# Kernel optimization log

Hardware: AMD Instinct MI355X
Metric: run time of the kernel (lower is better)

## Reference

```python
import jax, jax.numpy as jnp
import numpy as np

N_NODES = 100000
N_EDGES = 1600000
IN_SIZE = 256
HID = 64
HEADS = 2
OUT_SIZE = 16


def _gat_layer(x, W, a_l, a_r, b, src, dst, n_nodes, heads, feat):
    # x: [N, Din]; W: [Din, H*F]; a_l, a_r: [H, F]; b: [H*F]
    h = (x @ W).reshape(n_nodes, heads, feat)          # [N, H, F]
    el = jnp.sum(h * a_l, axis=-1)                     # [N, H]
    er = jnp.sum(h * a_r, axis=-1)                     # [N, H]
    e = jax.nn.leaky_relu(el[src] + er[dst], 0.2)      # [E, H]
    # segment softmax over incoming edges of each dst node
    m = jax.ops.segment_max(e, dst, num_segments=n_nodes)
    m = jnp.where(jnp.isfinite(m), m, 0.0)             # nodes with no in-edges
    p = jnp.exp(e - m[dst])                            # [E, H]
    s = jax.ops.segment_sum(p, dst, num_segments=n_nodes)
    alpha = p / (s[dst] + 1e-9)                        # [E, H]
    # scatter-add weighted source features
    out = jax.ops.segment_sum(alpha[:, :, None] * h[src], dst, num_segments=n_nodes)
    return out + b.reshape(1, heads, feat)             # [N, H, F]


def setup_inputs() -> dict:
    key = jax.random.key(0)
    ks = jax.random.split(key, 12)
    features = jax.random.normal(ks[0], (N_NODES, IN_SIZE), dtype=jnp.float32)
    src = jax.random.randint(ks[1], (N_EDGES,), 0, N_NODES, dtype=jnp.int32)
    dst = jax.random.randint(ks[2], (N_EDGES,), 0, N_NODES, dtype=jnp.int32)
    s1 = 1.0 / np.sqrt(IN_SIZE)
    s2 = 1.0 / np.sqrt(HID * HEADS)
    W1 = jax.random.normal(ks[3], (IN_SIZE, HEADS * HID), dtype=jnp.float32) * s1
    al1 = jax.random.normal(ks[4], (HEADS, HID), dtype=jnp.float32) * 0.1
    ar1 = jax.random.normal(ks[5], (HEADS, HID), dtype=jnp.float32) * 0.1
    b1 = jnp.zeros((HEADS * HID,), dtype=jnp.float32)
    W2 = jax.random.normal(ks[6], (HEADS * HID, HEADS * HID), dtype=jnp.float32) * s2
    al2 = jax.random.normal(ks[7], (HEADS, HID), dtype=jnp.float32) * 0.1
    ar2 = jax.random.normal(ks[8], (HEADS, HID), dtype=jnp.float32) * 0.1
    b2 = jnp.zeros((HEADS * HID,), dtype=jnp.float32)
    Wl = jax.random.normal(ks[9], (HEADS * HID, OUT_SIZE), dtype=jnp.float32) * s2
    bl = jnp.zeros((OUT_SIZE,), dtype=jnp.float32)
    return {"features": features, "src": src, "dst": dst,
            "W1": W1, "al1": al1, "ar1": ar1, "b1": b1,
            "W2": W2, "al2": al2, "ar2": ar2, "b2": b2,
            "Wl": Wl, "bl": bl}


def reference(features, src, dst, W1, al1, ar1, b1, W2, al2, ar2, b2, Wl, bl):
    n = features.shape[0]
    h = _gat_layer(features, W1, al1, ar1, b1.reshape(HEADS, HID).reshape(-1),
                   src, dst, n, HEADS, HID)
    h = jax.nn.elu(h.reshape(n, HEADS * HID))          # flatten(1) + ELU (dropout: eval)
    h = _gat_layer(h, W2, al2, ar2, b2, src, dst, n, HEADS, HID)
    h = jax.nn.elu(h.reshape(n, HEADS * HID))
    return h @ Wl + bl                                  # [N, OUT_SIZE]
```

## Files before the change

### kernel.cpp

```cpp
#include <hip/hip_runtime.h>
#include <hip/hip_fp16.h>

#define N_NODES 100000
#define N_EDGES 1600000
#define IN_SIZE 256
#define HID 64
#define HEADS 2
#define DMODEL 128
#define OUT_SZ 16

#define BSHIFT 9
#define BNODES 512
#define NB 196
#define CAP 16384
#define EPB 4096

typedef _Float16 f16x4 __attribute__((ext_vector_type(4)));
typedef _Float16 f16x8 __attribute__((ext_vector_type(8)));
typedef float f32x4 __attribute__((ext_vector_type(4)));


__global__ __launch_bounds__(256) void bin_kernel(const int* __restrict__ src,
                                                  const int* __restrict__ dst,
                                                  int* __restrict__ counts,
                                                  int2* __restrict__ bucketbuf, int e) {
    __shared__ int hist[NB];
    __shared__ int base[NB];
    int tid = threadIdx.x;
    int start = blockIdx.x * EPB;
    for (int i = tid; i < NB; i += 256) hist[i] = 0;
    __syncthreads();
    int pack[16];
    #pragma unroll
    for (int i = 0; i < 16; i++) {
        int idx = start + i * 256 + tid;
        int p = -1;
        if (idx < e) {
            int b = dst[idx] >> BSHIFT;
            int r = atomicAdd(&hist[b], 1);
            p = (b << 16) | r;
        }
        pack[i] = p;
    }
    __syncthreads();
    for (int i = tid; i < NB; i += 256)
        base[i] = atomicAdd(&counts[i], hist[i]);
    __syncthreads();
    #pragma unroll
    for (int i = 0; i < 16; i++) {
        int idx = start + i * 256 + tid;
        int p = pack[i];
        if (p >= 0) {
            int b = p >> 16;
            int pos = base[b] + (p & 0xffff);
            if (pos < CAP)
                bucketbuf[(size_t)b * CAP + pos] = make_int2(src[idx], dst[idx]);
        }
    }
}

__global__ void bucket_scan_kernel(const int* __restrict__ counts,
                                   int* __restrict__ bases) {
    __shared__ int lds[256];
    int tid = threadIdx.x;
    int t = (tid < NB) ? min(counts[tid], CAP) : 0;
    lds[tid] = t;
    __syncthreads();
    for (int off = 1; off < 256; off <<= 1) {
        int x = 0;
        if (tid >= off) x = lds[tid - off];
        __syncthreads();
        lds[tid] += x;
        __syncthreads();
    }
    if (tid < NB) bases[tid] = lds[tid] - t;
}


__global__ __launch_bounds__(256) void csr_kernel(const int2* __restrict__ bucketbuf,
                                                  const int* __restrict__ counts,
                                                  const int* __restrict__ bases,
                                                  int* __restrict__ deg,
                                                  int* __restrict__ offs,
                                                  int2* __restrict__ spack, int n) {
    __shared__ int hist[BNODES];
    __shared__ int cursor[BNODES];
    __shared__ int lds[256];
    int b = blockIdx.x;
    int tid = threadIdx.x;
    int cnt = min(counts[b], CAP);
    int base = bases[b];
    int node0 = b << BSHIFT;
    const int2* ebuf = bucketbuf + (size_t)b * CAP;

    hist[tid] = 0;
    hist[tid + 256] = 0;
    __syncthreads();
    for (int i = tid; i < cnt; i += 256)
        atomicAdd(&hist[ebuf[i].y - node0], 1);
    __syncthreads();

    int h0 = hist[2 * tid], h1 = hist[2 * tid + 1];
    lds[tid] = h0 + h1;
    __syncthreads();
    for (int off = 1; off < 256; off <<= 1) {
        int x = 0;
        if (tid >= off) x = lds[tid - off];
        __syncthreads();
        lds[tid] += x;
        __syncthreads();
    }
    int excl = lds[tid] - (h0 + h1);
    cursor[2 * tid] = excl;
    cursor[2 * tid + 1] = excl + h0;
    int g0 = node0 + 2 * tid, g1 = g0 + 1;
    if (g0 < n) { deg[g0] = h0; offs[g0] = base + excl; }
    if (g1 < n) { deg[g1] = h1; offs[g1] = base + excl + h0; }
    __syncthreads();

    for (int i = tid; i < cnt; i += 256) {
        int2 ed = ebuf[i];
        int p = atomicAdd(&cursor[ed.y - node0], 1);
        spack[base + p] = ed;
    }
}


template <int K>
__global__ void wt_kernel(const float* __restrict__ W, _Float16* __restrict__ Wt) {
    int i = blockIdx.x * blockDim.x + threadIdx.x;
    if (i >= 128 * K) return;
    int nr = i / K;
    int k = i - nr * K;
    Wt[i] = (_Float16)W[(size_t)k * 128 + nr];
}


template <int K, bool F16IN>
__global__ __launch_bounds__(256) void gemm_attn_kernel(const void* __restrict__ Ap,
                                                        const _Float16* __restrict__ Wt,
                                                        const float* __restrict__ al,
                                                        const float* __restrict__ ar,
                                                        uint32_t* __restrict__ h16,
                                                        float* __restrict__ el,
                                                        float* __restrict__ er, int n) {
    __shared__ _Float16 As[64 * 72];
    __shared__ _Float16 Bs[128 * 72];
    int tid = threadIdx.x;
    int w = tid >> 6;
    int lane = tid & 63;
    int c = lane & 15;
    int quad = lane >> 4;
    int r0 = blockIdx.x * 64;

    f32x4 acc[8];
    #pragma unroll
    for (int t = 0; t < 8; t++) acc[t] = (f32x4){0.f, 0.f, 0.f, 0.f};

    for (int kt = 0; kt < K; kt += 64) {
        {
            int lr = tid >> 4;
            int lc = (tid & 15) * 4;
            #pragma unroll
            for (int q = 0; q < 4; q++) {
                int row = lr + 16 * q;
                int gr = r0 + row;
                if constexpr (F16IN) {
                    const uint32_t* Af = (const uint32_t*)Ap;
                    uint2 v = make_uint2(0u, 0u);
                    if (gr < n) v = *(const uint2*)(Af + (size_t)gr * (K / 2) + (kt + lc) / 2);
                    *(uint2*)(As + row * 72 + lc) = v;
                } else {
                    const float* Af = (const float*)Ap;
                    float4 v = make_float4(0.f, 0.f, 0.f, 0.f);
                    if (gr < n) v = *(const float4*)(Af + (size_t)gr * K + kt + lc);
                    f16x4 hv = {(_Float16)v.x, (_Float16)v.y, (_Float16)v.z, (_Float16)v.w};
                    *(f16x4*)(As + row * 72 + lc) = hv;
                }
            }
            int nr = tid >> 1;
            int kc = (tid & 1) * 32;
            const uint4* gsrc = (const uint4*)(Wt + (size_t)nr * K + kt + kc);
            uint4 v0 = gsrc[0];
            uint4 v1 = gsrc[1];
            uint4 v2 = gsrc[2];
            uint4 v3 = gsrc[3];
            *(uint4*)(Bs + nr * 72 + kc + 0)  = v0;
            *(uint4*)(Bs + nr * 72 + kc + 8)  = v1;
            *(uint4*)(Bs + nr * 72 + kc + 16) = v2;
            *(uint4*)(Bs + nr * 72 + kc + 24) = v3;
        }
        __syncthreads();

        #pragma unroll
        for (int kk = 0; kk < 64; kk += 32) {
            f16x8 a = *(const f16x8*)(As + (16 * w + c) * 72 + kk + quad * 8);
            #pragma unroll
            for (int t = 0; t < 8; t++) {
                f16x8 b = *(const f16x8*)(Bs + (16 * t + c) * 72 + kk + quad * 8);
                acc[t] = __builtin_amdgcn_mfma_f32_16x16x32_f16(a, b, acc[t], 0, 0, 0);
            }
        }
        __syncthreads();
    }

    #pragma unroll
    for (int i = 0; i < 4; i++) {
        int gr = r0 + 16 * w + quad * 4 + i;
        float el0 = 0.f, el1 = 0.f, er0 = 0.f, er1 = 0.f;
        #pragma unroll
        for (int t = 0; t < 8; t++) {
            float hv = acc[t][i];
            float alv = al[16 * t + c];
            float arv = ar[16 * t + c];
            if (t < 4) { el0 += hv * alv; er0 += hv * arv; }
            else       { el1 += hv * alv; er1 += hv * arv; }
        }
        #pragma unroll
        for (int off = 1; off < 16; off <<= 1) {
            el0 += __shfl_xor(el0, off);
            el1 += __shfl_xor(el1, off);
            er0 += __shfl_xor(er0, off);
            er1 += __shfl_xor(er1, off);
        }
        if (c == 0 && gr < n) {
            *(float2*)(el + 2 * gr) = make_float2(el0, el1);
            *(float2*)(er + 2 * gr) = make_float2(er0, er1);
        }
        #pragma unroll
        for (int t = 0; t < 8; t++) {
            float own = acc[t][i];
            float other = __shfl_xor(own, 1);
            if ((c & 1) == 0 && gr < n) {
                __half2 hh = __floats2half2_rn(own, other);
                h16[(size_t)gr * 64 + 8 * t + (c >> 1)] = *(const uint32_t*)&hh;
            }
        }
    }
}


__global__ __launch_bounds__(256) void edge_w_kernel(const int2* __restrict__ spack,
                                                     const float* __restrict__ el,
                                                     const float* __restrict__ er,
                                                     int2* __restrict__ epack, int e) {
    int i = blockIdx.x * blockDim.x + threadIdx.x;
    if (i >= e) return;
    int2 sd = spack[i];
    float2 l = *(const float2*)(el + 2 * sd.x);
    float2 r = *(const float2*)(er + 2 * sd.y);
    float e0 = l.x + r.x; e0 = e0 >= 0.f ? e0 : 0.2f * e0;
    float e1 = l.y + r.y; e1 = e1 >= 0.f ? e1 : 0.2f * e1;
    __half2 wh = __floats2half2_rn(__expf(e0), __expf(e1));
    epack[i] = make_int2(sd.x, *(const int*)&wh);
}


__global__ __launch_bounds__(256) void agg_kernel(const uint32_t* __restrict__ hb,
                                                  const int2* __restrict__ epack,
                                                  const float* __restrict__ bias,
                                                  const int* __restrict__ offs,
                                                  const int* __restrict__ deg,
                                                  uint32_t* __restrict__ out16, int n) {
    int wid = (blockIdx.x * blockDim.x + threadIdx.x) >> 6;
    int lane = threadIdx.x & 63;
    if (wid >= n) return;
    int start = offs[wid];
    int d = deg[wid];
    int head = lane >> 5;

    float psum = 0.f, a0 = 0.f, a1 = 0.f;
    int j = 0;
    for (; j + 4 <= d; j += 4) {
        int2 p0 = epack[start + j + 0];
        int2 p1 = epack[start + j + 1];
        int2 p2 = epack[start + j + 2];
        int2 p3 = epack[start + j + 3];
        uint32_t u0 = hb[(size_t)p0.x * 64 + lane];
        uint32_t u1 = hb[(size_t)p1.x * 64 + lane];
        uint32_t u2 = hb[(size_t)p2.x * 64 + lane];
        uint32_t u3 = hb[(size_t)p3.x * 64 + lane];
        float2 wf0 = __half22float2(*(const __half2*)&p0.y);
        float2 wf1 = __half22float2(*(const __half2*)&p1.y);
        float2 wf2 = __half22float2(*(const __half2*)&p2.y);
        float2 wf3 = __half22float2(*(const __half2*)&p3.y);
        float w0 = head ? wf0.y : wf0.x;
        float w1 = head ? wf1.y : wf1.x;
        float w2 = head ? wf2.y : wf2.x;
        float w3 = head ? wf3.y : wf3.x;
        float2 h0 = __half22float2(*(const __half2*)&u0);
        float2 h1 = __half22float2(*(const __half2*)&u1);
        float2 h2 = __half22float2(*(const __half2*)&u2);
        float2 h3 = __half22float2(*(const __half2*)&u3);
        psum += (w0 + w1) + (w2 + w3);
        a0 += w0 * h0.x + w1 * h1.x + w2 * h2.x + w3 * h3.x;
        a1 += w0 * h0.y + w1 * h1.y + w2 * h2.y + w3 * h3.y;
    }
    for (; j < d; j++) {
        int2 p = epack[start + j];
        uint32_t u = hb[(size_t)p.x * 64 + lane];
        float2 wf = __half22float2(*(const __half2*)&p.y);
        float w = head ? wf.y : wf.x;
        float2 hv = __half22float2(*(const __half2*)&u);
        psum += w;
        a0 += w * hv.x;
        a1 += w * hv.y;
    }

    float inv = 1.f / (psum + 1e-9f);
    float2 bv = *(const float2*)(bias + 2 * lane);
    float o0 = a0 * inv + bv.x, o1 = a1 * inv + bv.y;
    o0 = o0 > 0.f ? o0 : (__expf(o0) - 1.f);
    o1 = o1 > 0.f ? o1 : (__expf(o1) - 1.f);
    __half2 oh = __floats2half2_rn(o0, o1);
    out16[(size_t)wid * 64 + lane] = *(const uint32_t*)&oh;
}


__global__ __launch_bounds__(256) void final_kernel(const uint32_t* __restrict__ x16,
                                                    const float* __restrict__ Wl,
                                                    const float* __restrict__ bl,
                                                    float* __restrict__ out, int n) {
    __shared__ float Ws[DMODEL * OUT_SZ];
    __shared__ float bs[OUT_SZ];
    int tid = threadIdx.x;
    for (int i = tid; i < DMODEL * OUT_SZ / 4; i += 256)
        ((float4*)Ws)[i] = ((const float4*)Wl)[i];
    if (tid < OUT_SZ) bs[tid] = bl[tid];
    __syncthreads();
    int node = blockIdx.x * 16 + (tid >> 4);
    int c = tid & 15;
    if (node >= n) return;
    const uint2* xr = (const uint2*)(x16 + (size_t)node * 64);
    float acc = bs[c];
    #pragma unroll
    for (int kk = 0; kk < 32; kk++) {
        uint2 v = xr[kk];
        float2 f0 = __half22float2(*(const __half2*)&v.x);
        float2 f1 = __half22float2(*(const __half2*)&v.y);
        acc += f0.x * Ws[(4 * kk + 0) * OUT_SZ + c];
        acc += f0.y * Ws[(4 * kk + 1) * OUT_SZ + c];
        acc += f1.x * Ws[(4 * kk + 2) * OUT_SZ + c];
        acc += f1.y * Ws[(4 * kk + 3) * OUT_SZ + c];
    }
    out[(size_t)node * OUT_SZ + c] = acc;
}


extern "C" void kernel_launch(void* const* d_in, const int* in_sizes, int n_in,
                              void* d_out, int out_size, void* d_ws, size_t ws_size,
                              hipStream_t stream) {
    const float* features = (const float*)d_in[0];
    const int*   src      = (const int*)d_in[1];
    const int*   dst      = (const int*)d_in[2];
    const float* W1  = (const float*)d_in[3];
    const float* al1 = (const float*)d_in[4];
    const float* ar1 = (const float*)d_in[5];
    const float* b1  = (const float*)d_in[6];
    const float* W2  = (const float*)d_in[7];
    const float* al2 = (const float*)d_in[8];
    const float* ar2 = (const float*)d_in[9];
    const float* b2  = (const float*)d_in[10];
    const float* Wl  = (const float*)d_in[11];
    const float* bl  = (const float*)d_in[12];
    float* out = (float*)d_out;

    const int n = N_NODES, e = N_EDGES;

    char* w = (char*)d_ws;
    uint32_t* h16 = (uint32_t*)w;       w += (size_t)n * 64 * 4;
    uint32_t* x1  = (uint32_t*)w;       w += (size_t)n * 64 * 4;
    uint32_t* x2  = (uint32_t*)w;       w += 26 * 1024 * 1024;
    float* el   = (float*)w;            w += (size_t)n * 2 * 4;
    float* er   = (float*)w;            w += (size_t)n * 2 * 4;
    int* deg    = (int*)w;              w += 400128;
    int* offs   = (int*)w;              w += 400128;
    int2* spack = (int2*)w;             w += (size_t)e * 8;
    int2* epack = (int2*)w;             w += (size_t)e * 8;
    int* counts = (int*)w;              w += 1024;
    int* bases  = (int*)w;              w += 1024;
    _Float16* Wt1 = (_Float16*)w;       w += 128 * IN_SIZE * 2;
    _Float16* Wt2 = (_Float16*)w;       w += 128 * DMODEL * 2;
    int2* bucketbuf = (int2*)x2;

    const int binBlocks = (e + EPB - 1) / EPB;
    const int eBlocks = (e + 255) / 256;
    const int gemmBlocks = (n + 63) / 64;
    const int nodeWaveBlocks = (n + 3) / 4;
    const int finalBlocks = (n + 15) / 16;

    hipMemsetAsync(counts, 0, NB * 4, stream);
    bin_kernel<<<binBlocks, 256, 0, stream>>>(src, dst, counts, bucketbuf, e);
    bucket_scan_kernel<<<1, 256, 0, stream>>>(counts, bases);
    csr_kernel<<<NB, 256, 0, stream>>>(bucketbuf, counts, bases, deg, offs, spack, n);

    wt_kernel<IN_SIZE><<<(128 * IN_SIZE + 255) / 256, 256, 0, stream>>>(W1, Wt1);
    wt_kernel<DMODEL><<<(128 * DMODEL + 255) / 256, 256, 0, stream>>>(W2, Wt2);

    gemm_attn_kernel<IN_SIZE, false><<<gemmBlocks, 256, 0, stream>>>(features, Wt1, al1, ar1,
                                                                     h16, el, er, n);
    edge_w_kernel<<<eBlocks, 256, 0, stream>>>(spack, el, er, epack, e);
    agg_kernel<<<nodeWaveBlocks, 256, 0, stream>>>(h16, epack, b1, offs, deg, x1, n);

    gemm_attn_kernel<DMODEL, true><<<gemmBlocks, 256, 0, stream>>>(x1, Wt2, al2, ar2,
                                                                   h16, el, er, n);
    edge_w_kernel<<<eBlocks, 256, 0, stream>>>(spack, el, er, epack, e);
    agg_kernel<<<nodeWaveBlocks, 256, 0, stream>>>(h16, epack, b2, offs, deg, x2, n);

    final_kernel<<<finalBlocks, 256, 0, stream>>>(x2, Wl, bl, out, n);

    (void)in_sizes; (void)n_in; (void)out_size; (void)ws_size;
}
```

Measured before the change: 470.6 us.

## Fuse edge-weight computation into aggregation and gather 16-byte rows per edge group

Removes the separate edge_w kernel and computes leaky-relu/exp attention weights inside the aggregation kernel from el/er, so the CSR stores only source indices (4 bytes per edge instead of 8). The aggregation wave now splits into 4 edge groups of 16 lanes, each lane loading 16 bytes (8 fp16 features) per edge, with a cross-group shuffle reduction at the end and a masked tail instead of a scalar remainder loop. This cuts two launches and the epack write/read traffic, and issues fewer, wider gathers. In exchange, el is gathered once per lane per edge and each wave only has four edge rows in flight at a time.

```diff
diff --git a/kernel.cpp b/kernel.cpp
--- a/kernel.cpp
+++ b/kernel.cpp
@@ -82,7 +82,7 @@
                                                   const int* __restrict__ bases,
                                                   int* __restrict__ deg,
                                                   int* __restrict__ offs,
-                                                  int2* __restrict__ spack, int n) {
+                                                  int* __restrict__ ssrc, int n) {
     __shared__ int hist[BNODES];
     __shared__ int cursor[BNODES];
     __shared__ int lds[256];
@@ -121,7 +121,7 @@
     for (int i = tid; i < cnt; i += 256) {
         int2 ed = ebuf[i];
         int p = atomicAdd(&cursor[ed.y - node0], 1);
-        spack[base + p] = ed;
+        ssrc[base + p] = ed.x;
     }
 }
 
@@ -240,24 +240,24 @@
 }
 
 
-__global__ __launch_bounds__(256) void edge_w_kernel(const int2* __restrict__ spack,
-                                                     const float* __restrict__ el,
-                                                     const float* __restrict__ er,
-                                                     int2* __restrict__ epack, int e) {
-    int i = blockIdx.x * blockDim.x + threadIdx.x;
-    if (i >= e) return;
-    int2 sd = spack[i];
-    float2 l = *(const float2*)(el + 2 * sd.x);
-    float2 r = *(const float2*)(er + 2 * sd.y);
-    float e0 = l.x + r.x; e0 = e0 >= 0.f ? e0 : 0.2f * e0;
-    float e1 = l.y + r.y; e1 = e1 >= 0.f ? e1 : 0.2f * e1;
-    __half2 wh = __floats2half2_rn(__expf(e0), __expf(e1));
-    epack[i] = make_int2(sd.x, *(const int*)&wh);
-}
-
+__device__ __forceinline__ float edge_w(float2 e, float erh, int head) {
+    float x = (head ? e.y : e.x) + erh;
+    x = x >= 0.f ? x : 0.2f * x;
+    return __expf(x);
+}
+
+__device__ __forceinline__ void acc8(uint4 u, float w, float* a) {
+    union { uint4 u4; f16x8 h8; } cv;
+    cv.u4 = u;
+    #pragma unroll
+    for (int i = 0; i < 8; i++)
+        a[i] = fmaf((float)cv.h8[i], w, a[i]);
+}
 
 __global__ __launch_bounds__(256) void agg_kernel(const uint32_t* __restrict__ hb,
-                                                  const int2* __restrict__ epack,
+                                                  const int* __restrict__ ssrc,
+                                                  const float* __restrict__ el,
+                                                  const float* __restrict__ er,
                                                   const float* __restrict__ bias,
                                                   const int* __restrict__ offs,
                                                   const int* __restrict__ deg,
@@ -267,53 +267,106 @@
     if (wid >= n) return;
     int start = offs[wid];
     int d = deg[wid];
-    int head = lane >> 5;
-
-    float psum = 0.f, a0 = 0.f, a1 = 0.f;
+    int g = lane >> 4;
+    int fl = lane & 15;
+    int head = fl >> 3;
+
+    float2 erv = *(const float2*)(er + 2 * wid);
+    float erh = head ? erv.y : erv.x;
+
+    const int* sp = ssrc + start;
+    const float2* el2 = (const float2*)el;
+    const char* hbb = (const char*)hb;
+    uint32_t foff = (uint32_t)(fl << 4);
+
+    float a[8];
+    #pragma unroll
+    for (int i = 0; i < 8; i++) a[i] = 0.f;
+    float psum = 0.f;
+
     int j = 0;
-    for (; j + 4 <= d; j += 4) {
-        int2 p0 = epack[start + j + 0];
-        int2 p1 = epack[start + j + 1];
-        int2 p2 = epack[start + j + 2];
-        int2 p3 = epack[start + j + 3];
-        uint32_t u0 = hb[(size_t)p0.x * 64 + lane];
-        uint32_t u1 = hb[(size_t)p1.x * 64 + lane];
-        uint32_t u2 = hb[(size_t)p2.x * 64 + lane];
-        uint32_t u3 = hb[(size_t)p3.x * 64 + lane];
-        float2 wf0 = __half22float2(*(const __half2*)&p0.y);
-        float2 wf1 = __half22float2(*(const __half2*)&p1.y);
-        float2 wf2 = __half22float2(*(const __half2*)&p2.y);
-        float2 wf3 = __half22float2(*(const __half2*)&p3.y);
-        float w0 = head ? wf0.y : wf0.x;
-        float w1 = head ? wf1.y : wf1.x;
-        float w2 = head ? wf2.y : wf2.x;
-        float w3 = head ? wf3.y : wf3.x;
-        float2 h0 = __half22float2(*(const __half2*)&u0);
-        float2 h1 = __half22float2(*(const __half2*)&u1);
-        float2 h2 = __half22float2(*(const __half2*)&u2);
-        float2 h3 = __half22float2(*(const __half2*)&u3);
+    for (; j + 16 <= d; j += 16) {
+        int s0 = sp[j + g];
+        int s1 = sp[j + 4 + g];
+        int s2 = sp[j + 8 + g];
+        int s3 = sp[j + 12 + g];
+        float2 e0 = el2[s0];
+        uint4 u0 = *(const uint4*)(hbb + (((uint32_t)s0 << 8) + foff));
+        float2 e1 = el2[s1];
+        uint4 u1 = *(const uint4*)(hbb + (((uint32_t)s1 << 8) + foff));
+        float2 e2 = el2[s2];
+        uint4 u2 = *(const uint4*)(hbb + (((uint32_t)s2 << 8) + foff));
+        float2 e3 = el2[s3];
+        uint4 u3 = *(const uint4*)(hbb + (((uint32_t)s3 << 8) + foff));
+        float w0 = edge_w(e0, erh, head);
+        float w1 = edge_w(e1, erh, head);
+        float w2 = edge_w(e2, erh, head);
+        float w3 = edge_w(e3, erh, head);
         psum += (w0 + w1) + (w2 + w3);
-        a0 += w0 * h0.x + w1 * h1.x + w2 * h2.x + w3 * h3.x;
-        a1 += w0 * h0.y + w1 * h1.y + w2 * h2.y + w3 * h3.y;
-    }
-    for (; j < d; j++) {
-        int2 p = epack[start + j];
-        uint32_t u = hb[(size_t)p.x * 64 + lane];
-        float2 wf = __half22float2(*(const __half2*)&p.y);
-        float w = head ? wf.y : wf.x;
-        float2 hv = __half22float2(*(const __half2*)&u);
-        psum += w;
-        a0 += w * hv.x;
-        a1 += w * hv.y;
-    }
-
-    float inv = 1.f / (psum + 1e-9f);
-    float2 bv = *(const float2*)(bias + 2 * lane);
-    float o0 = a0 * inv + bv.x, o1 = a1 * inv + bv.y;
-    o0 = o0 > 0.f ? o0 : (__expf(o0) - 1.f);
-    o1 = o1 > 0.f ? o1 : (__expf(o1) - 1.f);
-    __half2 oh = __floats2half2_rn(o0, o1);
-    out16[(size_t)wid * 64 + lane] = *(const uint32_t*)&oh;
+        acc8(u0, w0, a);
+        acc8(u1, w1, a);
+        acc8(u2, w2, a);
+        acc8(u3, w3, a);
+    }
+    if (j < d) {
+        int last = d - 1;
+        int i0 = j + g,      i1 = j + 4 + g, i2 = j + 8 + g, i3 = j + 12 + g;
+        int c0 = min(i0, last), c1 = min(i1, last), c2 = min(i2, last), c3 = min(i3, last);
+        int s0 = sp[c0];
+        int s1 = sp[c1];
+        int s2 = sp[c2];
+        int s3 = sp[c3];
+        float2 e0 = el2[s0];
+        uint4 u0 = *(const uint4*)(hbb + (((uint32_t)s0 << 8) + foff));
+        float2 e1 = el2[s1];
+        uint4 u1 = *(const uint4*)(hbb + (((uint32_t)s1 << 8) + foff));
+        float2 e2 = el2[s2];
+        uint4 u2 = *(const uint4*)(hbb + (((uint32_t)s2 << 8) + foff));
+        float2 e3 = el2[s3];
+        uint4 u3 = *(const uint4*)(hbb + (((uint32_t)s3 << 8) + foff));
+        float w0 = (i0 <= last) ? edge_w(e0, erh, head) : 0.f;
+        float w1 = (i1 <= last) ? edge_w(e1, erh, head) : 0.f;
+        float w2 = (i2 <= last) ? edge_w(e2, erh, head) : 0.f;
+        float w3 = (i3 <= last) ? edge_w(e3, erh, head) : 0.f;
+        psum += (w0 + w1) + (w2 + w3);
+        acc8(u0, w0, a);
+        acc8(u1, w1, a);
+        acc8(u2, w2, a);
+        acc8(u3, w3, a);
+    }
+
+    #pragma unroll
+    for (int i = 0; i < 8; i++) {
+        a[i] += __shfl_xor(a[i], 16);
+        a[i] += __shfl_xor(a[i], 32);
+    }
+    psum += __shfl_xor(psum, 16);
+    psum += __shfl_xor(psum, 32);
+
+    if (lane < 16) {
+        float inv = 1.f / (psum + 1e-9f);
+        float4 b0 = *(const float4*)(bias + 8 * lane);
+        float4 b1 = *(const float4*)(bias + 8 * lane + 4);
+        float o[8];
+        o[0] = fmaf(a[0], inv, b0.x);
+        o[1] = fmaf(a[1], inv, b0.y);
+        o[2] = fmaf(a[2], inv, b0.z);
+        o[3] = fmaf(a[3], inv, b0.w);
+        o[4] = fmaf(a[4], inv, b1.x);
+        o[5] = fmaf(a[5], inv, b1.y);
+        o[6] = fmaf(a[6], inv, b1.z);
+        o[7] = fmaf(a[7], inv, b1.w);
+        #pragma unroll
+        for (int i = 0; i < 8; i++)
+            o[i] = o[i] > 0.f ? o[i] : (__expf(o[i]) - 1.f);
+        __half2 h01 = __floats2half2_rn(o[0], o[1]);
+        __half2 h23 = __floats2half2_rn(o[2], o[3]);
+        __half2 h45 = __floats2half2_rn(o[4], o[5]);
+        __half2 h67 = __floats2half2_rn(o[6], o[7]);
+        uint4 ov = make_uint4(*(const uint32_t*)&h01, *(const uint32_t*)&h23,
+                              *(const uint32_t*)&h45, *(const uint32_t*)&h67);
+        ((uint4*)(out16 + (size_t)wid * 64))[lane] = ov;
+    }
 }
 
 
@@ -375,8 +428,7 @@
     float* er   = (float*)w;            w += (size_t)n * 2 * 4;
     int* deg    = (int*)w;              w += 400128;
     int* offs   = (int*)w;              w += 400128;
-    int2* spack = (int2*)w;             w += (size_t)e * 8;
-    int2* epack = (int2*)w;             w += (size_t)e * 8;
+    int* ssrc   = (int*)w;              w += (size_t)e * 4;
     int* counts = (int*)w;              w += 1024;
     int* bases  = (int*)w;              w += 1024;
     _Float16* Wt1 = (_Float16*)w;       w += 128 * IN_SIZE * 2;
@@ -384,7 +436,6 @@
     int2* bucketbuf = (int2*)x2;
 
     const int binBlocks = (e + EPB - 1) / EPB;
-    const int eBlocks = (e + 255) / 256;
     const int gemmBlocks = (n + 63) / 64;
     const int nodeWaveBlocks = (n + 3) / 4;
     const int finalBlocks = (n + 15) / 16;
@@ -392,20 +443,18 @@
     hipMemsetAsync(counts, 0, NB * 4, stream);
     bin_kernel<<<binBlocks, 256, 0, stream>>>(src, dst, counts, bucketbuf, e);
     bucket_scan_kernel<<<1, 256, 0, stream>>>(counts, bases);
-    csr_kernel<<<NB, 256, 0, stream>>>(bucketbuf, counts, bases, deg, offs, spack, n);
+    csr_kernel<<<NB, 256, 0, stream>>>(bucketbuf, counts, bases, deg, offs, ssrc, n);
 
     wt_kernel<IN_SIZE><<<(128 * IN_SIZE + 255) / 256, 256, 0, stream>>>(W1, Wt1);
     wt_kernel<DMODEL><<<(128 * DMODEL + 255) / 256, 256, 0, stream>>>(W2, Wt2);
 
     gemm_attn_kernel<IN_SIZE, false><<<gemmBlocks, 256, 0, stream>>>(features, Wt1, al1, ar1,
                                                                      h16, el, er, n);
-    edge_w_kernel<<<eBlocks, 256, 0, stream>>>(spack, el, er, epack, e);
-    agg_kernel<<<nodeWaveBlocks, 256, 0, stream>>>(h16, epack, b1, offs, deg, x1, n);
+    agg_kernel<<<nodeWaveBlocks, 256, 0, stream>>>(h16, ssrc, el, er, b1, offs, deg, x1, n);
 
     gemm_attn_kernel<DMODEL, true><<<gemmBlocks, 256, 0, stream>>>(x1, Wt2, al2, ar2,
                                                                    h16, el, er, n);
-    edge_w_kernel<<<eBlocks, 256, 0, stream>>>(spack, el, er, epack, e);
-    agg_kernel<<<nodeWaveBlocks, 256, 0, stream>>>(h16, epack, b2, offs, deg, x2, n);
+    agg_kernel<<<nodeWaveBlocks, 256, 0, stream>>>(h16, ssrc, el, er, b2, offs, deg, x2, n);
 
     final_kernel<<<finalBlocks, 256, 0, stream>>>(x2, Wl, bl, out, n);
 
```

Result: faster. 434.8 us (-7.6%).
